# Kernel optimization log

Hardware: AMD Instinct MI355X
Metric: run time of the kernel (lower is better)

Reference implementation:

```python
import jax, jax.numpy as jnp
import numpy as np

N_FEAT = 1024
N_HIDDEN = 31


def _lstm_cell(x, h, c, W_ih, W_hh, b_ih, b_hh):
    # PyTorch LSTMCell: gates ordered i, f, g, o
    gates = x @ W_ih.T + b_ih + h @ W_hh.T + b_hh
    i, f, g, o = jnp.split(gates, 4, axis=-1)
    i = jax.nn.sigmoid(i)
    f = jax.nn.sigmoid(f)
    g = jnp.tanh(g)
    o = jax.nn.sigmoid(o)
    c_new = f * c + i * g
    h_new = o * jnp.tanh(c_new)
    return h_new, c_new


def setup_inputs() -> dict:
    key = jax.random.key(0)
    ks = jax.random.split(key, 12)
    B, T = 64, 512
    s1 = 1.0 / np.sqrt(N_HIDDEN)
    inp = {
        "input": jax.random.normal(ks[0], (B, T, N_FEAT), dtype=jnp.float32),
        "W_ih1": jax.random.uniform(ks[1], (4 * N_HIDDEN, N_FEAT), jnp.float32, -s1, s1),
        "W_hh1": jax.random.uniform(ks[2], (4 * N_HIDDEN, N_HIDDEN), jnp.float32, -s1, s1),
        "b_ih1": jax.random.uniform(ks[3], (4 * N_HIDDEN,), jnp.float32, -s1, s1),
        "b_hh1": jax.random.uniform(ks[4], (4 * N_HIDDEN,), jnp.float32, -s1, s1),
        "W_ih2": jax.random.uniform(ks[5], (4 * N_HIDDEN, N_HIDDEN), jnp.float32, -s1, s1),
        "W_hh2": jax.random.uniform(ks[6], (4 * N_HIDDEN, N_HIDDEN), jnp.float32, -s1, s1),
        "b_ih2": jax.random.uniform(ks[7], (4 * N_HIDDEN,), jnp.float32, -s1, s1),
        "b_hh2": jax.random.uniform(ks[8], (4 * N_HIDDEN,), jnp.float32, -s1, s1),
        "W_lin": jax.random.uniform(ks[9], (N_FEAT, N_HIDDEN), jnp.float32, -s1, s1),
        "b_lin": jax.random.uniform(ks[10], (N_FEAT,), jnp.float32, -s1, s1),
        "future": 16,
    }
    return inp


def reference(input, W_ih1, W_hh1, b_ih1, b_hh1, W_ih2, W_hh2, b_ih2, b_hh2, W_lin, b_lin, future):
    B = input.shape[0]
    h0 = jnp.zeros((B, N_HIDDEN), dtype=input.dtype)
    state0 = (h0, h0, h0, h0)  # h_t, c_t, h_t2, c_t2

    def step(state, x_t):
        h_t, c_t, h_t2, c_t2 = state
        h_t, c_t = _lstm_cell(x_t, h_t, c_t, W_ih1, W_hh1, b_ih1, b_hh1)
        h_t2, c_t2 = _lstm_cell(h_t, h_t2, c_t2, W_ih2, W_hh2, b_ih2, b_hh2)
        out = h_t2 @ W_lin.T + b_lin  # [B, N_FEAT]
        return (h_t, c_t, h_t2, c_t2), out

    # teacher-forced pass over the given sequence
    xs = jnp.swapaxes(input, 0, 1)  # [T, B, F]
    state, outs = jax.lax.scan(step, state0, xs)
    last = outs[-1]

    def fut_step(carry, _):
        state, out = carry
        state, out = step(state, out)
        return (state, out), out

    if future > 0:
        _, fut_outs = jax.lax.scan(fut_step, (state, last), None, length=future)
        outs = jnp.concatenate([outs, fut_outs], axis=0)

    return jnp.swapaxes(outs, 0, 1)  # [B, T+future, N_FEAT]
```

## Files before the change

### kernel.cpp

```cpp
#include <hip/hip_runtime.h>
#include <hip/hip_bf16.h>

#define BB_  64
#define TT_  512
#define FF_  1024
#define HH_  31
#define GG_  124
#define FUT_ 16
#define TTOT_ 528
#define OUT_ROW_ ((size_t)TTOT_ * FF_)

#define PRE1_OFF ((size_t)0)
#define H2A_OFF  (PRE1_OFF + (size_t)TT_*64*128)
#define WT_OFF   (H2A_OFF  + (size_t)TTOT_*64*32)
#define MV_OFF   (WT_OFF   + 31*1024)

__device__ __forceinline__ float rdlane(float v, int k) {
    return __uint_as_float(__builtin_amdgcn_readlane(__float_as_uint(v), k));
}

#define REP31(M) M(0) M(1) M(2) M(3) M(4) M(5) M(6) M(7) M(8) M(9) \
                 M(10) M(11) M(12) M(13) M(14) M(15) M(16) M(17) M(18) M(19) \
                 M(20) M(21) M(22) M(23) M(24) M(25) M(26) M(27) M(28) M(29) M(30)

__global__ void k0_prep(const float* __restrict__ Wlin, float* __restrict__ WT) {
    int i = blockIdx.x * 256 + threadIdx.x;
    int j = i / 31;
    int k = i - j * 31;
    WT[k * 1024 + j] = Wlin[i];
}

__global__ __launch_bounds__(64) void k0b_mv(
    const float* __restrict__ Wih1, const float* __restrict__ Wlin,
    const float* __restrict__ blin, float* __restrict__ Mv)
{
    int i = blockIdx.x * 64 + threadIdx.x;
    int g = i >> 5, k = i & 31;
    const float* wr = Wih1 + (size_t)g * FF_;
    float acc = 0.0f;
    if (k < 31) {
#pragma unroll 8
        for (int j = 0; j < FF_; j++) acc += wr[j] * Wlin[j * 31 + k];
    } else {
#pragma unroll 8
        for (int j = 0; j < FF_; j++) acc += wr[j] * blin[j];
    }
    Mv[i] = acc;
}

__global__ __launch_bounds__(256) void k1_pregate(
    const float* __restrict__ X,
    const float* __restrict__ Wih1,
    const float* __restrict__ bih1,
    const float* __restrict__ bhh1,
    float* __restrict__ pre1)
{
    __shared__ __align__(16) float xs[32][64];
    __shared__ __align__(16) float ws[32][128];
    const int tid  = threadIdx.x;
    const int t    = blockIdx.x;
    const int tcol = tid & 31, trow = tid >> 5;
    const int c0 = tcol * 4, r0 = trow * 8;

    float4 acc[8];
#pragma unroll
    for (int r = 0; r < 8; r++) acc[r] = make_float4(0.f, 0.f, 0.f, 0.f);

    for (int kc = 0; kc < 32; ++kc) {
        const int k0 = kc * 32;
#pragma unroll
        for (int p = 0; p < 2; p++) {
            int i = tid + p * 256;
            int r = i >> 3, f = i & 7;
            float4 v = *(const float4*)(X + (size_t)r * TT_ * FF_ + (size_t)t * FF_ + k0 + f * 4);
            xs[f * 4 + 0][r] = v.x; xs[f * 4 + 1][r] = v.y;
            xs[f * 4 + 2][r] = v.z; xs[f * 4 + 3][r] = v.w;
        }
#pragma unroll
        for (int p = 0; p < 4; p++) {
            int i = tid + p * 256;
            int g = i >> 3, f = i & 7;
            float4 v = make_float4(0.f, 0.f, 0.f, 0.f);
            if (g < GG_) v = *(const float4*)(Wih1 + (size_t)g * FF_ + k0 + f * 4);
            ws[f * 4 + 0][g] = v.x; ws[f * 4 + 1][g] = v.y;
            ws[f * 4 + 2][g] = v.z; ws[f * 4 + 3][g] = v.w;
        }
        __syncthreads();
#pragma unroll
        for (int k = 0; k < 32; k++) {
            float4 wv = *(const float4*)&ws[k][c0];
            float4 xa = *(const float4*)&xs[k][r0];
            float4 xb = *(const float4*)&xs[k][r0 + 4];
            float rx[8] = {xa.x, xa.y, xa.z, xa.w, xb.x, xb.y, xb.z, xb.w};
#pragma unroll
            for (int r = 0; r < 8; r++) {
                acc[r].x += rx[r] * wv.x; acc[r].y += rx[r] * wv.y;
                acc[r].z += rx[r] * wv.z; acc[r].w += rx[r] * wv.w;
            }
        }
        __syncthreads();
    }
    float bias[4];
#pragma unroll
    for (int cc = 0; cc < 4; cc++) {
        int c = c0 + cc;
        bias[cc] = (c < GG_) ? (bih1[c] + bhh1[c]) : 0.0f;
    }
#pragma unroll
    for (int r = 0; r < 8; r++) {
        int m = t * 64 + r0 + r;
        float4 o = acc[r];
        o.x += bias[0]; o.y += bias[1]; o.z += bias[2]; o.w += bias[3];
        *(float4*)(pre1 + (size_t)m * 128 + c0) = o;
    }
}

__global__ __launch_bounds__(128, 1) void k2_recur(
    const float* __restrict__ pre1,
    const float* __restrict__ Whh1,
    const float* __restrict__ Wih2,
    const float* __restrict__ Whh2,
    const float* __restrict__ bih1, const float* __restrict__ bhh1,
    const float* __restrict__ bih2, const float* __restrict__ bhh2,
    const float* __restrict__ Mv,
    float* __restrict__ h2a)
{
    __shared__ float gA[2][128];
    __shared__ float g2[2][128];
    const int L  = threadIdx.x;
    const int bb = blockIdx.x;
    const int j  = L & 63;
    const int gc = (L < GG_) ? L : (GG_ - 1);
    const bool isg = (gc >= 62 && gc < 93);
    const bool own = (j < HH_);

#define WLOAD(k) float w1_##k  = Whh1[gc * 31 + k]; \
                 float wi2_##k = Wih2[gc * 31 + k]; \
                 float wh2_##k = Whh2[gc * 31 + k];
    REP31(WLOAD)
#undef WLOAD

    const float b2c = bih2[gc] + bhh2[gc];

    float hv1 = 0.0f, cv1 = 0.0f, hv2 = 0.0f, cv2 = 0.0f;

    float cur0 = pre1[(size_t)bb * 128 + L];
    float pnxt = pre1[((size_t)1 * 64 + bb) * 128 + L];
    {
        float a = cur0;
#define DOTP(k) { float hk = rdlane(hv1, k); a += w1_##k * hk; }
        REP31(DOTP)
#undef DOTP
        float z = isg ? (2.0f * a) : a;
        float s = 1.0f / (1.0f + __expf(-z));
        gA[1][L] = isg ? (2.0f * s - 1.0f) : s;
    }
    __syncthreads();
    if (own) {
        float ig = gA[1][j];
        float fg = gA[1][j + 31];
        float gg = gA[1][j + 62];
        float og = gA[1][j + 93];
        cv1 = fg * cv1 + ig * gg;
        float e = __expf(-2.0f * cv1);
        hv1 = og * (2.0f / (1.0f + e) - 1.0f);
    }

    for (int t = 0; t < TT_ - 1; t++) {
        const int pb = t & 1;
        const float cur = pnxt;
        float pld = 0.0f;
        if (t + 2 < TT_) pld = pre1[((size_t)(t + 2) * 64 + bb) * 128 + L];

        float b = b2c;
        float a = cur;
#define DOTM(k) { float h1k = rdlane(hv1, k); float h2k = rdlane(hv2, k); \
                  b += wi2_##k * h1k + wh2_##k * h2k; \
                  a += w1_##k * h1k; }
        REP31(DOTM)
#undef DOTM
        {
            float z = isg ? (2.0f * b) : b;
            float s = 1.0f / (1.0f + __expf(-z));
            g2[pb][L] = isg ? (2.0f * s - 1.0f) : s;
        }
        {
            float z = isg ? (2.0f * a) : a;
            float s = 1.0f / (1.0f + __expf(-z));
            gA[pb][L] = isg ? (2.0f * s - 1.0f) : s;
        }
        __syncthreads();
        if (own) {
            float ig = g2[pb][j];
            float fg = g2[pb][j + 31];
            float gg = g2[pb][j + 62];
            float og = g2[pb][j + 93];
            cv2 = fg * cv2 + ig * gg;
            float e = __expf(-2.0f * cv2);
            hv2 = og * (2.0f / (1.0f + e) - 1.0f);
            float i1 = gA[pb][j];
            float f1 = gA[pb][j + 31];
            float g1v = gA[pb][j + 62];
            float o1 = gA[pb][j + 93];
            cv1 = f1 * cv1 + i1 * g1v;
            float e1 = __expf(-2.0f * cv1);
            hv1 = o1 * (2.0f / (1.0f + e1) - 1.0f);
        }
        if (L < HH_) h2a[((size_t)t * 64 + bb) * 32 + L] = hv2;
        pnxt = pld;
    }

    {
        float b = b2c;
#define DOTT(k) { float h1k = rdlane(hv1, k); float h2k = rdlane(hv2, k); \
                  b += wi2_##k * h1k + wh2_##k * h2k; }
        REP31(DOTT)
#undef DOTT
        float z = isg ? (2.0f * b) : b;
        float s = 1.0f / (1.0f + __expf(-z));
        g2[1][L] = isg ? (2.0f * s - 1.0f) : s;
    }
    __syncthreads();
    if (own) {
        float ig = g2[1][j];
        float fg = g2[1][j + 31];
        float gg = g2[1][j + 62];
        float og = g2[1][j + 93];
        cv2 = fg * cv2 + ig * gg;
        float e = __expf(-2.0f * cv2);
        hv2 = og * (2.0f / (1.0f + e) - 1.0f);
    }
    if (L < HH_) h2a[((size_t)(TT_ - 1) * 64 + bb) * 32 + L] = hv2;

#define MLOAD(k) float m_##k = Mv[gc * 32 + k];
    REP31(MLOAD)
#undef MLOAD
    float m_31 = Mv[gc * 32 + 31];
    const float b1c = bih1[gc] + bhh1[gc];

    for (int sft = 0; sft < FUT_; sft++) {
        float a = b1c + m_31;
#define DOTF1(k) { float h2k = rdlane(hv2, k); a += m_##k * h2k; }
        REP31(DOTF1)
#undef DOTF1
#define DOTF2(k) { float hk = rdlane(hv1, k); a += w1_##k * hk; }
        REP31(DOTF2)
#undef DOTF2
        {
            float z = isg ? (2.0f * a) : a;
            float s = 1.0f / (1.0f + __expf(-z));
            gA[0][L] = isg ? (2.0f * s - 1.0f) : s;
        }
        __syncthreads();
        if (own) {
            float ig = gA[0][j];
            float fg = gA[0][j + 31];
            float gg = gA[0][j + 62];
            float og = gA[0][j + 93];
            cv1 = fg * cv1 + ig * gg;
            float e = __expf(-2.0f * cv1);
            hv1 = og * (2.0f / (1.0f + e) - 1.0f);
        }
        float b = b2c;
#define DOTF3(k) { float h1k = rdlane(hv1, k); float h2k = rdlane(hv2, k); \
                   b += wi2_##k * h1k + wh2_##k * h2k; }
        REP31(DOTF3)
#undef DOTF3
        {
            float z = isg ? (2.0f * b) : b;
            float s = 1.0f / (1.0f + __expf(-z));
            g2[0][L] = isg ? (2.0f * s - 1.0f) : s;
        }
        __syncthreads();
        if (own) {
            float ig = g2[0][j];
            float fg = g2[0][j + 31];
            float gg = g2[0][j + 62];
            float og = g2[0][j + 93];
            cv2 = fg * cv2 + ig * gg;
            float e = __expf(-2.0f * cv2);
            hv2 = og * (2.0f / (1.0f + e) - 1.0f);
        }
        if (L < HH_) h2a[((size_t)(TT_ + sft) * 64 + bb) * 32 + L] = hv2;
    }
}

__global__ __launch_bounds__(256) void k3_outlin(
    const float* __restrict__ h2a,
    const float* __restrict__ WT,
    const float* __restrict__ blin,
    float* __restrict__ out)
{
    __shared__ __align__(16) float hl[16][32];
    const int tid = threadIdx.x;
    const int m0  = blockIdx.x * 16;
#pragma unroll
    for (int p = 0; p < 2; p++) {
        int i = tid + p * 256;
        int r = i >> 5, k = i & 31;
        hl[r][k] = h2a[(size_t)(m0 + r) * 32 + k];
    }
    __syncthreads();
    const int c0 = tid * 4;
    float4 bl = *(const float4*)(blin + c0);
    float4 acc[16];
#pragma unroll
    for (int r = 0; r < 16; r++) acc[r] = bl;
    for (int k = 0; k < 31; k++) {
        float4 wv = *(const float4*)(WT + k * 1024 + c0);
#pragma unroll
        for (int r = 0; r < 16; r++) {
            float h = hl[r][k];
            acc[r].x += h * wv.x; acc[r].y += h * wv.y;
            acc[r].z += h * wv.z; acc[r].w += h * wv.w;
        }
    }
    const int t  = m0 >> 6;
    const int b0 = m0 & 63;
#pragma unroll
    for (int r = 0; r < 16; r++) {
        int b = b0 + r;
        *(float4*)(out + (size_t)b * OUT_ROW_ + (size_t)t * FF_ + c0) = acc[r];
    }
}

extern "C" void kernel_launch(void* const* d_in, const int* in_sizes, int n_in,
                              void* d_out, int out_size, void* d_ws, size_t ws_size,
                              hipStream_t stream) {
    (void)in_sizes; (void)n_in; (void)out_size; (void)ws_size;
    const float* X    = (const float*)d_in[0];
    const float* Wih1 = (const float*)d_in[1];
    const float* Whh1 = (const float*)d_in[2];
    const float* bih1 = (const float*)d_in[3];
    const float* bhh1 = (const float*)d_in[4];
    const float* Wih2 = (const float*)d_in[5];
    const float* Whh2 = (const float*)d_in[6];
    const float* bih2 = (const float*)d_in[7];
    const float* bhh2 = (const float*)d_in[8];
    const float* Wlin = (const float*)d_in[9];
    const float* blin = (const float*)d_in[10];

    float* ws   = (float*)d_ws;
    float* pre1 = ws + PRE1_OFF;
    float* h2a  = ws + H2A_OFF;
    float* WT   = ws + WT_OFF;
    float* Mv   = ws + MV_OFF;
    float* out  = (float*)d_out;

    hipLaunchKernelGGL(k0_prep,    dim3(124),  dim3(256), 0, stream, Wlin, WT);
    hipLaunchKernelGGL(k0b_mv,     dim3(62),   dim3(64),  0, stream, Wih1, Wlin, blin, Mv);
    hipLaunchKernelGGL(k1_pregate, dim3(TT_),  dim3(256), 0, stream, X, Wih1, bih1, bhh1, pre1);
    hipLaunchKernelGGL(k2_recur,   dim3(BB_),  dim3(128), 0, stream, pre1, Whh1, Wih2, Whh2,
                       bih1, bhh1, bih2, bhh2, Mv, h2a);
    hipLaunchKernelGGL(k3_outlin,  dim3(TTOT_*4), dim3(256), 0, stream, h2a, WT, blin, out);
}
```

Before: 832.1 us.

## Split recurrent dot products across two K-halves with shared-memory partial-sum reduction

The recurrent kernel now uses 256 threads per batch row instead of 128. Each pair of wavefronts computes partial gate pre-activations over half of the hidden dimension (16 taps instead of 31), and the partials are summed through LDS before the activations. This halves the serial readlane/FMA chain per step on the latency-bound recurrence. In exchange it adds LDS traffic, moves all gate nonlinearities onto the owner lanes, and uses a constant 1 in lane 31 of hv2 so the Mv bias column (m_31) is picked up inside the dot product.

```diff
diff --git a/kernel.cpp b/kernel.cpp
--- a/kernel.cpp
+++ b/kernel.cpp
@@ -19,9 +19,8 @@
     return __uint_as_float(__builtin_amdgcn_readlane(__float_as_uint(v), k));
 }
 
-#define REP31(M) M(0) M(1) M(2) M(3) M(4) M(5) M(6) M(7) M(8) M(9) \
-                 M(10) M(11) M(12) M(13) M(14) M(15) M(16) M(17) M(18) M(19) \
-                 M(20) M(21) M(22) M(23) M(24) M(25) M(26) M(27) M(28) M(29) M(30)
+#define REP16(M) M(0) M(1) M(2) M(3) M(4) M(5) M(6) M(7) \
+                 M(8) M(9) M(10) M(11) M(12) M(13) M(14) M(15)
 
 __global__ void k0_prep(const float* __restrict__ Wlin, float* __restrict__ WT) {
     int i = blockIdx.x * 256 + threadIdx.x;
@@ -115,7 +114,7 @@
     }
 }
 
-__global__ __launch_bounds__(128, 1) void k2_recur(
+__global__ __launch_bounds__(256, 1) void k2_recur(
     const float* __restrict__ pre1,
     const float* __restrict__ Whh1,
     const float* __restrict__ Wih2,
@@ -125,84 +124,94 @@
     const float* __restrict__ Mv,
     float* __restrict__ h2a)
 {
-    __shared__ float gA[2][128];
-    __shared__ float g2[2][128];
-    const int L  = threadIdx.x;
-    const int bb = blockIdx.x;
-    const int j  = L & 63;
-    const int gc = (L < GG_) ? L : (GG_ - 1);
-    const bool isg = (gc >= 62 && gc < 93);
+    __shared__ float pbuf[2][2][2][128];
+    const int L    = threadIdx.x;
+    const int bb   = blockIdx.x;
+    const int wid  = L >> 6;
+    const int j    = L & 63;
+    const int half = wid >> 1;
+    const int gl   = (wid & 1) * 64 + j;
+    const int g    = (gl < GG_) ? gl : (GG_ - 1);
     const bool own = (j < HH_);
-
-#define WLOAD(k) float w1_##k  = Whh1[gc * 31 + k]; \
-                 float wi2_##k = Wih2[gc * 31 + k]; \
-                 float wh2_##k = Whh2[gc * 31 + k];
-    REP31(WLOAD)
+    const int KLO  = half * 16;
+
+#define WLOAD(i) float w1_##i  = (KLO + i < HH_) ? Whh1[g * 31 + KLO + i] : 0.0f; \
+                 float wi2_##i = (KLO + i < HH_) ? Wih2[g * 31 + KLO + i] : 0.0f; \
+                 float wh2_##i = (KLO + i < HH_) ? Whh2[g * 31 + KLO + i] : 0.0f;
+    REP16(WLOAD)
 #undef WLOAD
-
-    const float b2c = bih2[gc] + bhh2[gc];
-
-    float hv1 = 0.0f, cv1 = 0.0f, hv2 = 0.0f, cv2 = 0.0f;
-
-    float cur0 = pre1[(size_t)bb * 128 + L];
-    float pnxt = pre1[((size_t)1 * 64 + bb) * 128 + L];
-    {
-        float a = cur0;
-#define DOTP(k) { float hk = rdlane(hv1, k); a += w1_##k * hk; }
-        REP31(DOTP)
-#undef DOTP
-        float z = isg ? (2.0f * a) : a;
-        float s = 1.0f / (1.0f + __expf(-z));
-        gA[1][L] = isg ? (2.0f * s - 1.0f) : s;
-    }
+#define WPIN(i) asm("" : "+v"(w1_##i), "+v"(wi2_##i), "+v"(wh2_##i));
+    REP16(WPIN)
+#undef WPIN
+
+    const float b2c = (half == 0) ? (bih2[g] + bhh2[g]) : 0.0f;
+    const float b1c = (half == 0) ? (bih1[g] + bhh1[g]) : 0.0f;
+
+    float hv1 = 0.0f, cv1 = 0.0f, cv2 = 0.0f;
+    float hv2 = (j == 31) ? 1.0f : 0.0f;
+
+    float cur0 = 0.0f, pnxt = 0.0f;
+    if (half == 0) {
+        cur0 = pre1[(size_t)bb * 128 + gl];
+        pnxt = pre1[((size_t)64 + bb) * 128 + gl];
+    }
+
+    pbuf[1][0][half][gl] = (half == 0) ? cur0 : 0.0f;
     __syncthreads();
     if (own) {
-        float ig = gA[1][j];
-        float fg = gA[1][j + 31];
-        float gg = gA[1][j + 62];
-        float og = gA[1][j + 93];
-        cv1 = fg * cv1 + ig * gg;
-        float e = __expf(-2.0f * cv1);
-        hv1 = og * (2.0f / (1.0f + e) - 1.0f);
+        float ai = pbuf[1][0][0][j]      + pbuf[1][0][1][j];
+        float af = pbuf[1][0][0][j + 31] + pbuf[1][0][1][j + 31];
+        float ag = pbuf[1][0][0][j + 62] + pbuf[1][0][1][j + 62];
+        float ao = pbuf[1][0][0][j + 93] + pbuf[1][0][1][j + 93];
+        float i1 = 1.0f / (1.0f + __expf(-ai));
+        float f1 = 1.0f / (1.0f + __expf(-af));
+        float s1 = 1.0f / (1.0f + __expf(-2.0f * ag));
+        float g1 = 2.0f * s1 - 1.0f;
+        float o1 = 1.0f / (1.0f + __expf(-ao));
+        cv1 = f1 * cv1 + i1 * g1;
+        float e1 = __expf(-2.0f * cv1);
+        hv1 = o1 * (2.0f / (1.0f + e1) - 1.0f);
     }
 
     for (int t = 0; t < TT_ - 1; t++) {
-        const int pb = t & 1;
+        const int par = t & 1;
         const float cur = pnxt;
         float pld = 0.0f;
-        if (t + 2 < TT_) pld = pre1[((size_t)(t + 2) * 64 + bb) * 128 + L];
-
-        float b = b2c;
-        float a = cur;
-#define DOTM(k) { float h1k = rdlane(hv1, k); float h2k = rdlane(hv2, k); \
-                  b += wi2_##k * h1k + wh2_##k * h2k; \
-                  a += w1_##k * h1k; }
-        REP31(DOTM)
+        if (half == 0 && t + 2 < TT_) pld = pre1[((size_t)(t + 2) * 64 + bb) * 128 + gl];
+
+        float pb = b2c;
+        float pa = (half == 0) ? cur : 0.0f;
+#define DOTM(i) { float h1k = rdlane(hv1, KLO + i); float h2k = rdlane(hv2, KLO + i); \
+                  pb += wi2_##i * h1k + wh2_##i * h2k; \
+                  pa += w1_##i * h1k; }
+        REP16(DOTM)
 #undef DOTM
-        {
-            float z = isg ? (2.0f * b) : b;
-            float s = 1.0f / (1.0f + __expf(-z));
-            g2[pb][L] = isg ? (2.0f * s - 1.0f) : s;
-        }
-        {
-            float z = isg ? (2.0f * a) : a;
-            float s = 1.0f / (1.0f + __expf(-z));
-            gA[pb][L] = isg ? (2.0f * s - 1.0f) : s;
-        }
+        pbuf[par][1][half][gl] = pb;
+        pbuf[par][0][half][gl] = pa;
         __syncthreads();
         if (own) {
-            float ig = g2[pb][j];
-            float fg = g2[pb][j + 31];
-            float gg = g2[pb][j + 62];
-            float og = g2[pb][j + 93];
+            float bi = pbuf[par][1][0][j]      + pbuf[par][1][1][j];
+            float bf = pbuf[par][1][0][j + 31] + pbuf[par][1][1][j + 31];
+            float bg = pbuf[par][1][0][j + 62] + pbuf[par][1][1][j + 62];
+            float bo = pbuf[par][1][0][j + 93] + pbuf[par][1][1][j + 93];
+            float ig = 1.0f / (1.0f + __expf(-bi));
+            float fg = 1.0f / (1.0f + __expf(-bf));
+            float sg = 1.0f / (1.0f + __expf(-2.0f * bg));
+            float gg = 2.0f * sg - 1.0f;
+            float og = 1.0f / (1.0f + __expf(-bo));
             cv2 = fg * cv2 + ig * gg;
-            float e = __expf(-2.0f * cv2);
-            hv2 = og * (2.0f / (1.0f + e) - 1.0f);
-            float i1 = gA[pb][j];
-            float f1 = gA[pb][j + 31];
-            float g1v = gA[pb][j + 62];
-            float o1 = gA[pb][j + 93];
-            cv1 = f1 * cv1 + i1 * g1v;
+            float e2 = __expf(-2.0f * cv2);
+            hv2 = og * (2.0f / (1.0f + e2) - 1.0f);
+            float ai = pbuf[par][0][0][j]      + pbuf[par][0][1][j];
+            float af = pbuf[par][0][0][j + 31] + pbuf[par][0][1][j + 31];
+            float ag = pbuf[par][0][0][j + 62] + pbuf[par][0][1][j + 62];
+            float ao = pbuf[par][0][0][j + 93] + pbuf[par][0][1][j + 93];
+            float i1 = 1.0f / (1.0f + __expf(-ai));
+            float f1 = 1.0f / (1.0f + __expf(-af));
+            float s1 = 1.0f / (1.0f + __expf(-2.0f * ag));
+            float g1 = 2.0f * s1 - 1.0f;
+            float o1 = 1.0f / (1.0f + __expf(-ao));
+            cv1 = f1 * cv1 + i1 * g1;
             float e1 = __expf(-2.0f * cv1);
             hv1 = o1 * (2.0f / (1.0f + e1) - 1.0f);
         }
@@ -211,77 +220,83 @@
     }
 
     {
-        float b = b2c;
-#define DOTT(k) { float h1k = rdlane(hv1, k); float h2k = rdlane(hv2, k); \
-                  b += wi2_##k * h1k + wh2_##k * h2k; }
-        REP31(DOTT)
+        float pb = b2c;
+#define DOTT(i) { float h1k = rdlane(hv1, KLO + i); float h2k = rdlane(hv2, KLO + i); \
+                  pb += wi2_##i * h1k + wh2_##i * h2k; }
+        REP16(DOTT)
 #undef DOTT
-        float z = isg ? (2.0f * b) : b;
-        float s = 1.0f / (1.0f + __expf(-z));
-        g2[1][L] = isg ? (2.0f * s - 1.0f) : s;
+        pbuf[1][1][half][gl] = pb;
     }
     __syncthreads();
     if (own) {
-        float ig = g2[1][j];
-        float fg = g2[1][j + 31];
-        float gg = g2[1][j + 62];
-        float og = g2[1][j + 93];
+        float bi = pbuf[1][1][0][j]      + pbuf[1][1][1][j];
+        float bf = pbuf[1][1][0][j + 31] + pbuf[1][1][1][j + 31];
+        float bg = pbuf[1][1][0][j + 62] + pbuf[1][1][1][j + 62];
+        float bo = pbuf[1][1][0][j + 93] + pbuf[1][1][1][j + 93];
+        float ig = 1.0f / (1.0f + __expf(-bi));
+        float fg = 1.0f / (1.0f + __expf(-bf));
+        float sg = 1.0f / (1.0f + __expf(-2.0f * bg));
+        float gg = 2.0f * sg - 1.0f;
+        float og = 1.0f / (1.0f + __expf(-bo));
         cv2 = fg * cv2 + ig * gg;
-        float e = __expf(-2.0f * cv2);
-        hv2 = og * (2.0f / (1.0f + e) - 1.0f);
+        float e2 = __expf(-2.0f * cv2);
+        hv2 = og * (2.0f / (1.0f + e2) - 1.0f);
     }
     if (L < HH_) h2a[((size_t)(TT_ - 1) * 64 + bb) * 32 + L] = hv2;
 
-#define MLOAD(k) float m_##k = Mv[gc * 32 + k];
-    REP31(MLOAD)
+#define MLOAD(i) float m_##i = Mv[g * 32 + KLO + i];
+    REP16(MLOAD)
 #undef MLOAD
-    float m_31 = Mv[gc * 32 + 31];
-    const float b1c = bih1[gc] + bhh1[gc];
-
-    for (int sft = 0; sft < FUT_; sft++) {
-        float a = b1c + m_31;
-#define DOTF1(k) { float h2k = rdlane(hv2, k); a += m_##k * h2k; }
-        REP31(DOTF1)
-#undef DOTF1
-#define DOTF2(k) { float hk = rdlane(hv1, k); a += w1_##k * hk; }
-        REP31(DOTF2)
-#undef DOTF2
-        {
-            float z = isg ? (2.0f * a) : a;
-            float s = 1.0f / (1.0f + __expf(-z));
-            gA[0][L] = isg ? (2.0f * s - 1.0f) : s;
-        }
+#define MPIN(i) asm("" : "+v"(m_##i));
+    REP16(MPIN)
+#undef MPIN
+
+    for (int s = 0; s < FUT_; s++) {
+        float pa = b1c;
+#define DF1(i) { float h2k = rdlane(hv2, KLO + i); pa += m_##i * h2k; }
+        REP16(DF1)
+#undef DF1
+#define DF2(i) { float h1k = rdlane(hv1, KLO + i); pa += w1_##i * h1k; }
+        REP16(DF2)
+#undef DF2
+        pbuf[0][0][half][gl] = pa;
         __syncthreads();
         if (own) {
-            float ig = gA[0][j];
-            float fg = gA[0][j + 31];
-            float gg = gA[0][j + 62];
-            float og = gA[0][j + 93];
-            cv1 = fg * cv1 + ig * gg;
-            float e = __expf(-2.0f * cv1);
-            hv1 = og * (2.0f / (1.0f + e) - 1.0f);
-        }
-        float b = b2c;
-#define DOTF3(k) { float h1k = rdlane(hv1, k); float h2k = rdlane(hv2, k); \
-                   b += wi2_##k * h1k + wh2_##k * h2k; }
-        REP31(DOTF3)
-#undef DOTF3
-        {
-            float z = isg ? (2.0f * b) : b;
-            float s = 1.0f / (1.0f + __expf(-z));
-            g2[0][L] = isg ? (2.0f * s - 1.0f) : s;
-        }
+            float ai = pbuf[0][0][0][j]      + pbuf[0][0][1][j];
+            float af = pbuf[0][0][0][j + 31] + pbuf[0][0][1][j + 31];
+            float ag = pbuf[0][0][0][j + 62] + pbuf[0][0][1][j + 62];
+            float ao = pbuf[0][0][0][j + 93] + pbuf[0][0][1][j + 93];
+            float i1 = 1.0f / (1.0f + __expf(-ai));
+            float f1 = 1.0f / (1.0f + __expf(-af));
+            float s1 = 1.0f / (1.0f + __expf(-2.0f * ag));
+            float g1 = 2.0f * s1 - 1.0f;
+            float o1 = 1.0f / (1.0f + __expf(-ao));
+            cv1 = f1 * cv1 + i1 * g1;
+            float e1 = __expf(-2.0f * cv1);
+            hv1 = o1 * (2.0f / (1.0f + e1) - 1.0f);
+        }
+        float pb = b2c;
+#define DF3(i) { float h1k = rdlane(hv1, KLO + i); float h2k = rdlane(hv2, KLO + i); \
+                 pb += wi2_##i * h1k + wh2_##i * h2k; }
+        REP16(DF3)
+#undef DF3
+        pbuf[0][1][half][gl] = pb;
         __syncthreads();
         if (own) {
-            float ig = g2[0][j];
-            float fg = g2[0][j + 31];
-            float gg = g2[0][j + 62];
-            float og = g2[0][j + 93];
+            float bi = pbuf[0][1][0][j]      + pbuf[0][1][1][j];
+            float bf = pbuf[0][1][0][j + 31] + pbuf[0][1][1][j + 31];
+            float bg = pbuf[0][1][0][j + 62] + pbuf[0][1][1][j + 62];
+            float bo = pbuf[0][1][0][j + 93] + pbuf[0][1][1][j + 93];
+            float ig = 1.0f / (1.0f + __expf(-bi));
+            float fg = 1.0f / (1.0f + __expf(-bf));
+            float sg = 1.0f / (1.0f + __expf(-2.0f * bg));
+            float gg = 2.0f * sg - 1.0f;
+            float og = 1.0f / (1.0f + __expf(-bo));
             cv2 = fg * cv2 + ig * gg;
-            float e = __expf(-2.0f * cv2);
-            hv2 = og * (2.0f / (1.0f + e) - 1.0f);
-        }
-        if (L < HH_) h2a[((size_t)(TT_ + sft) * 64 + bb) * 32 + L] = hv2;
+            float e2 = __expf(-2.0f * cv2);
+            hv2 = og * (2.0f / (1.0f + e2) - 1.0f);
+        }
+        if (L < HH_) h2a[((size_t)(TT_ + s) * 64 + bb) * 32 + L] = hv2;
     }
 }
 
@@ -350,7 +365,7 @@
     hipLaunchKernelGGL(k0_prep,    dim3(124),  dim3(256), 0, stream, Wlin, WT);
     hipLaunchKernelGGL(k0b_mv,     dim3(62),   dim3(64),  0, stream, Wih1, Wlin, blin, Mv);
     hipLaunchKernelGGL(k1_pregate, dim3(TT_),  dim3(256), 0, stream, X, Wih1, bih1, bhh1, pre1);
-    hipLaunchKernelGGL(k2_recur,   dim3(BB_),  dim3(128), 0, stream, pre1, Whh1, Wih2, Whh2,
+    hipLaunchKernelGGL(k2_recur,   dim3(BB_),  dim3(256), 0, stream, pre1, Whh1, Wih2, Whh2,
                        bih1, bhh1, bih2, bhh2, Mv, h2a);
     hipLaunchKernelGGL(k3_outlin,  dim3(TTOT_*4), dim3(256), 0, stream, h2a, WT, blin, out);
 }
```

Result: slower. 1.012 ms (+21.6%).
